# Kernel tuning notes

Hardware: AMD Instinct MI355X
Metric: run time of the kernel (lower is better)

## Reference

```python
import jax, jax.numpy as jnp
import numpy as np

B, S, D, H = 8, 1024, 1024, 16
DH = D // H


def setup_inputs() -> dict:
    key = jax.random.key(0)
    ks = jax.random.split(key, 7)
    scale = 1.0 / np.sqrt(DH)
    return {
        "sequences": jax.random.normal(ks[0], (B, S, D), dtype=jnp.float32),
        "Wq": jax.random.uniform(ks[1], (H, DH, DH), jnp.float32, -scale, scale),
        "bq": jax.random.uniform(ks[2], (H, DH), jnp.float32, -scale, scale),
        "Wk": jax.random.uniform(ks[3], (H, DH, DH), jnp.float32, -scale, scale),
        "bk": jax.random.uniform(ks[4], (H, DH), jnp.float32, -scale, scale),
        "Wv": jax.random.uniform(ks[5], (H, DH, DH), jnp.float32, -scale, scale),
        "bv": jax.random.uniform(ks[6], (H, DH), jnp.float32, -scale, scale),
    }


def reference(sequences, Wq, bq, Wk, bk, Wv, bv):
    # split channels into heads: [B,S,H,DH]
    x = sequences.reshape(B, S, H, DH)
    # per-head linear maps (torch Linear: y = x @ W.T + b)
    q = jnp.einsum("bshd,hed->bshe", x, Wq) + bq  # [B,S,H,DH]
    k = jnp.einsum("bshd,hed->bshe", x, Wk) + bk
    v = jnp.einsum("bshd,hed->bshe", x, Wv) + bv
    scores = jnp.einsum("bshd,bthd->bhst", q, k) / jnp.sqrt(jnp.asarray(DH, x.dtype))
    attn = jax.nn.softmax(scores, axis=-1)  # [B,H,S,S]
    out = jnp.einsum("bhst,bthd->bshd", attn, v)  # [B,S,H,DH]
    return out.reshape(B, S, D)
```

## Files before the change

kernel.cpp:

```cpp
#include <hip/hip_runtime.h>
#include <hip/hip_bf16.h>


constexpr int NB = 8, NS = 1024, ND = 1024, NH = 16, NDH = 64;

typedef __bf16 bf16x8 __attribute__((ext_vector_type(8)));
typedef float f32x4 __attribute__((ext_vector_type(4)));

__device__ __forceinline__ f32x4 mfma16(bf16x8 a, bf16x8 b, f32x4 c) {
  return __builtin_amdgcn_mfma_f32_16x16x32_bf16(a, b, c, 0, 0, 0);
}

__device__ __forceinline__ float fast_exp2(float x) {
#if __has_builtin(__builtin_amdgcn_exp2f)
  return __builtin_amdgcn_exp2f(x);
#else
  return __builtin_exp2f(x);
#endif
}

__device__ __forceinline__ unsigned pack2(float lo, float hi) {
  unsigned uh = __builtin_bit_cast(unsigned, hi) + 0x8000u;
  unsigned ul = __builtin_bit_cast(unsigned, lo) + 0x8000u;
  return __builtin_amdgcn_perm(uh, ul, 0x07060302u);
}

__device__ __forceinline__ unsigned pack2t(float lo, float hi) {
  return __builtin_amdgcn_perm(__builtin_bit_cast(unsigned, hi),
                               __builtin_bit_cast(unsigned, lo), 0x07060302u);
}

__device__ __forceinline__ bf16x8 cvt2bf8(float4 lo, float4 hi) {
  bf16x8 r;
  r[0] = (__bf16)lo.x; r[1] = (__bf16)lo.y; r[2] = (__bf16)lo.z; r[3] = (__bf16)lo.w;
  r[4] = (__bf16)hi.x; r[5] = (__bf16)hi.y; r[6] = (__bf16)hi.z; r[7] = (__bf16)hi.w;
  return r;
}

__device__ __forceinline__ void gload16(const __hip_bfloat16* g, __hip_bfloat16* l) {
  __builtin_amdgcn_global_load_lds(
      (const __attribute__((address_space(1))) void*)g,
      (__attribute__((address_space(3))) void*)l, 16, 0, 0);
}

__global__ __launch_bounds__(256) void qkv_proj_kernel(
    const float* __restrict__ x,
    const float* __restrict__ Wq, const float* __restrict__ bq,
    const float* __restrict__ Wk, const float* __restrict__ bk,
    const float* __restrict__ Wv, const float* __restrict__ bv,
    __hip_bfloat16* __restrict__ Qo, __hip_bfloat16* __restrict__ Ko,
    __hip_bfloat16* __restrict__ Vt) {
  __shared__ __align__(16) __hip_bfloat16 Wlds[3][NDH][72];
  const int tid = threadIdx.x;
  const int wave = tid >> 6, lane = tid & 63;
  const int m = lane & 15, quad = lane >> 4;
  const int h = blockIdx.x & (NH - 1);
  const int sblk = blockIdx.x >> 4;

  const float* Ws[3] = {Wq + h * 4096, Wk + h * 4096, Wv + h * 4096};
#pragma unroll
  for (int mt = 0; mt < 3; mt++) {
#pragma unroll
    for (int p = 0; p < 4; p++) {
      int idx = (p * 256 + tid) * 4;
      float4 v = *(const float4*)(Ws[mt] + idx);
      uint2 w;
      w.x = pack2(v.x, v.y);
      w.y = pack2(v.z, v.w);
      *(uint2*)&Wlds[mt][idx >> 6][idx & 63] = w;
    }
  }
  __syncthreads();

  float bq4[4][4], bk4[4][4], bvv[4];
#pragma unroll
  for (int nt = 0; nt < 4; nt++) {
    float4 a = *(const float4*)(bq + h * 64 + nt * 16 + quad * 4);
    float4 c = *(const float4*)(bk + h * 64 + nt * 16 + quad * 4);
    bq4[nt][0] = a.x; bq4[nt][1] = a.y; bq4[nt][2] = a.z; bq4[nt][3] = a.w;
    bk4[nt][0] = c.x; bk4[nt][1] = c.y; bk4[nt][2] = c.z; bk4[nt][3] = c.w;
    bvv[nt] = bv[h * 64 + nt * 16 + m];
  }

  const int rowbase = sblk * 256 + wave * 64;
  bf16x8 Xf[4][2];
#pragma unroll
  for (int st = 0; st < 4; st++) {
    const float* xp = x + (size_t)(rowbase + st * 16 + m) * ND + h * NDH + quad * 8;
#pragma unroll
    for (int c = 0; c < 2; c++) {
      float4 lo = *(const float4*)(xp + c * 32);
      float4 hi = *(const float4*)(xp + c * 32 + 4);
      Xf[st][c] = cvt2bf8(lo, hi);
    }
  }

  const int b = rowbase >> 10;
  const int s0 = rowbase & 1023;
  const float qscale = 0.18033688011112042f;

#pragma unroll
  for (int mt = 0; mt < 3; mt++) {
#pragma unroll
    for (int nt = 0; nt < 4; nt++) {
      bf16x8 w0 = *(const bf16x8*)&Wlds[mt][nt * 16 + m][quad * 8];
      bf16x8 w1 = *(const bf16x8*)&Wlds[mt][nt * 16 + m][32 + quad * 8];
#pragma unroll
      for (int st = 0; st < 4; st++) {
        f32x4 acc = {0.f, 0.f, 0.f, 0.f};
        if (mt < 2) {
          acc = mfma16(w0, Xf[st][0], acc);
          acc = mfma16(w1, Xf[st][1], acc);
          const int srow = s0 + st * 16 + m;
          uint2 w;
          if (mt == 0) {
            w.x = pack2((acc[0] + bq4[nt][0]) * qscale, (acc[1] + bq4[nt][1]) * qscale);
            w.y = pack2((acc[2] + bq4[nt][2]) * qscale, (acc[3] + bq4[nt][3]) * qscale);
            *(uint2*)(Qo + ((size_t)(b * NH + h) * NS + srow) * NDH +
                      nt * 16 + quad * 4) = w;
          } else {
            w.x = pack2(acc[0] + bk4[nt][0], acc[1] + bk4[nt][1]);
            w.y = pack2(acc[2] + bk4[nt][2], acc[3] + bk4[nt][3]);
            *(uint2*)(Ko + ((size_t)(b * NH + h) * NS + srow) * NDH +
                      nt * 16 + quad * 4) = w;
          }
        } else {
          acc = mfma16(Xf[st][0], w0, acc);
          acc = mfma16(Xf[st][1], w1, acc);
          uint2 w;
          w.x = pack2(acc[0] + bvv[nt], acc[1] + bvv[nt]);
          w.y = pack2(acc[2] + bvv[nt], acc[3] + bvv[nt]);
          *(uint2*)(Vt + ((size_t)(b * NH + h) * NDH + nt * 16 + m) * NS + s0 +
                    st * 16 + quad * 4) = w;
        }
      }
    }
  }
}

__global__ __launch_bounds__(256, 4) void attn_kernel(
    const __hip_bfloat16* __restrict__ Q,
    const __hip_bfloat16* __restrict__ K,
    const __hip_bfloat16* __restrict__ Vt,
    float* __restrict__ out) {
  __shared__ __align__(16) __hip_bfloat16 Kt[2][64][64];
  __shared__ __align__(16) __hip_bfloat16 Vl[2][64][64];

  const int tid = threadIdx.x;
  const int wave = tid >> 6, lane = tid & 63;
  const int m = lane & 15, quad = lane >> 4;

  const int xcd = blockIdx.x & 7;
  const int j = blockIdx.x >> 3;
  const int bh = xcd * 16 + (j & 15);
  const int qblk = j >> 4;
  const int qbase = qblk * 128 + wave * 32;

  const __hip_bfloat16* Qp = Q + (size_t)bh * NS * NDH;
  const __hip_bfloat16* Kp = K + (size_t)bh * NS * NDH;
  const __hip_bfloat16* Vp = Vt + (size_t)bh * NDH * NS;

  bf16x8 Bq[2][2];
#pragma unroll
  for (int g = 0; g < 2; g++)
#pragma unroll
    for (int dh = 0; dh < 2; dh++)
      Bq[g][dh] = *(const bf16x8*)(Qp + (size_t)(qbase + g * 16 + m) * NDH +
                                   dh * 32 + quad * 8);

  f32x4 accO[2][4];
  f32x4 lsum[2];
#pragma unroll
  for (int g = 0; g < 2; g++) {
    lsum[g] = (f32x4){0.f, 0.f, 0.f, 0.f};
#pragma unroll
    for (int nt = 0; nt < 4; nt++) accO[g][nt] = (f32x4){0.f, 0.f, 0.f, 0.f};
  }
  bf16x8 ones8;
#pragma unroll
  for (int i = 0; i < 8; i++) ones8[i] = (__bf16)1.0f;
  const f32x4 fzero = {0.f, 0.f, 0.f, 0.f};

  const int krow = 8 * (m >> 2) + (m & 3);
  const int fK = (m & 3) ^ (((m >> 2) & 1) << 2);
  const int kc0 = (quad ^ fK) * 8;
  const int vbase = quad ^ (m & 7);

#define STAGE(buf, tb)                                                        \
  {                                                                           \
    _Pragma("unroll") for (int l = 0; l < 2; l++) {                           \
      const int krb = wave * 16 + l * 8;                                      \
      const int csK = (lane & 7) ^ ((lane >> 3) & 3) ^ (l << 2);              \
      gload16(Kp + (size_t)((tb) * 64 + krb + (lane >> 3)) * NDH + csK * 8,   \
              &Kt[buf][krb][0]);                                              \
      const int vrb = wave * 16 + l * 8;                                      \
      const int csV = (lane & 7) ^ (lane >> 3);                               \
      gload16(Vp + (size_t)(vrb + (lane >> 3)) * NS + (tb) * 64 + csV * 8,    \
              &Vl[buf][vrb][0]);                                              \
    }                                                                         \
  }

  STAGE(0, 0);

  for (int tb = 0; tb < 16; tb++) {
    const int cur = tb & 1;
    __syncthreads();
    if (tb + 1 < 16) STAGE(cur ^ 1, tb + 1);

    bf16x8 Pa[2][2];
#pragma unroll
    for (int c = 0; c < 2; c++) {
      uint4 u[2];
#pragma unroll
      for (int p = 0; p < 2; p++) {
        const __hip_bfloat16* kr = &Kt[cur][c * 32 + 4 * p + krow][0];
        bf16x8 k0 = *(const bf16x8*)(kr + kc0);
        bf16x8 k1 = *(const bf16x8*)(kr + (kc0 ^ 32));
#pragma unroll
        for (int g = 0; g < 2; g++) {
          f32x4 a = mfma16(k1, Bq[g][1], mfma16(k0, Bq[g][0], fzero));
          unsigned w0 = pack2t(fast_exp2(a[0]), fast_exp2(a[1]));
          unsigned w1 = pack2t(fast_exp2(a[2]), fast_exp2(a[3]));
          if (p == 0) { u[g].x = w0; u[g].y = w1; }
          else        { u[g].z = w0; u[g].w = w1; }
        }
      }
#pragma unroll
      for (int g = 0; g < 2; g++) Pa[g][c] = __builtin_bit_cast(bf16x8, u[g]);
    }
    __builtin_amdgcn_s_setprio(1);
#pragma unroll
    for (int g = 0; g < 2; g++)
#pragma unroll
      for (int c = 0; c < 2; c++) lsum[g] = mfma16(Pa[g][c], ones8, lsum[g]);
#pragma unroll
    for (int nt = 0; nt < 4; nt++) {
#pragma unroll
      for (int c = 0; c < 2; c++) {
        const int off = (vbase ^ (c << 2)) << 3;
        bf16x8 v = *(const bf16x8*)&Vl[cur][nt * 16 + m][off];
#pragma unroll
        for (int g = 0; g < 2; g++)
          accO[g][nt] = mfma16(Pa[g][c], v, accO[g][nt]);
      }
    }
    __builtin_amdgcn_s_setprio(0);
  }
#undef STAGE

  const int b = bh >> 4, h = bh & (NH - 1);
#pragma unroll
  for (int g = 0; g < 2; g++) {
#pragma unroll
    for (int r = 0; r < 4; r++) {
      float inv = 1.0f / lsum[g][r];
      int srow = qbase + g * 16 + quad * 4 + r;
      float* op = out + (size_t)(b * NS + srow) * ND + h * NDH;
#pragma unroll
      for (int nt = 0; nt < 4; nt++) op[nt * 16 + m] = accO[g][nt][r] * inv;
    }
  }
}

extern "C" void kernel_launch(void* const* d_in, const int* in_sizes, int n_in,
                              void* d_out, int out_size, void* d_ws, size_t ws_size,
                              hipStream_t stream) {
  const float* x  = (const float*)d_in[0];
  const float* Wq = (const float*)d_in[1];
  const float* bq = (const float*)d_in[2];
  const float* Wk = (const float*)d_in[3];
  const float* bk = (const float*)d_in[4];
  const float* Wv = (const float*)d_in[5];
  const float* bv = (const float*)d_in[6];
  float* out = (float*)d_out;

  const size_t elems = (size_t)NB * NH * NS * NDH;
  __hip_bfloat16* Qw = (__hip_bfloat16*)d_ws;
  __hip_bfloat16* Kw = Qw + elems;
  __hip_bfloat16* Vw = Kw + elems;

  qkv_proj_kernel<<<512, 256, 0, stream>>>(x, Wq, bq, Wk, bk, Wv, bv, Qw, Kw, Vw);
  attn_kernel<<<1024, 256, 0, stream>>>(Qw, Kw, Vw, out);
}
```

Baseline: 141.4 us.

## Software-pipeline attention loop: overlap QK of next tile with PV of previous

Restructures the attention main loop so each tile's QK^T and exp phase runs while the PV accumulation consumes the previous tile's probabilities. The loop is unrolled by two with ping-pong probability registers, and V is triple-buffered in shared memory so it is not overwritten while still being read. The goal is to interleave exp/VALU work with MFMA work and hide shared-memory load latency. In exchange it holds more live registers, which can hurt occupancy under the 4-block launch bound, uses more LDS, and drops the s_setprio hints.

```diff
diff --git a/kernel.cpp b/kernel.cpp
--- a/kernel.cpp
+++ b/kernel.cpp
@@ -144,7 +144,7 @@
     const __hip_bfloat16* __restrict__ Vt,
     float* __restrict__ out) {
   __shared__ __align__(16) __hip_bfloat16 Kt[2][64][64];
-  __shared__ __align__(16) __hip_bfloat16 Vl[2][64][64];
+  __shared__ __align__(16) __hip_bfloat16 Vl[3][64][64];
 
   const int tid = threadIdx.x;
   const int wave = tid >> 6, lane = tid & 63;
@@ -186,67 +186,74 @@
   const int kc0 = (quad ^ fK) * 8;
   const int vbase = quad ^ (m & 7);
 
-#define STAGE(buf, tb)                                                        \
+#define STAGE(kb, vb, tb)                                                     \
   {                                                                           \
     _Pragma("unroll") for (int l = 0; l < 2; l++) {                           \
       const int krb = wave * 16 + l * 8;                                      \
       const int csK = (lane & 7) ^ ((lane >> 3) & 3) ^ (l << 2);              \
       gload16(Kp + (size_t)((tb) * 64 + krb + (lane >> 3)) * NDH + csK * 8,   \
-              &Kt[buf][krb][0]);                                              \
+              &Kt[kb][krb][0]);                                               \
       const int vrb = wave * 16 + l * 8;                                      \
       const int csV = (lane & 7) ^ (lane >> 3);                               \
       gload16(Vp + (size_t)(vrb + (lane >> 3)) * NS + (tb) * 64 + csV * 8,    \
-              &Vl[buf][vrb][0]);                                              \
+              &Vl[vb][vrb][0]);                                               \
     }                                                                         \
   }
 
-  STAGE(0, 0);
-
-  for (int tb = 0; tb < 16; tb++) {
-    const int cur = tb & 1;
+#define QK_PHASE(cur_, PaNew)                                                 \
+  {                                                                           \
+    _Pragma("unroll") for (int c = 0; c < 2; c++) {                           \
+      uint4 u[2];                                                             \
+      _Pragma("unroll") for (int p = 0; p < 2; p++) {                         \
+        const __hip_bfloat16* kr = &Kt[cur_][c * 32 + 4 * p + krow][0];       \
+        bf16x8 k0 = *(const bf16x8*)(kr + kc0);                               \
+        bf16x8 k1 = *(const bf16x8*)(kr + (kc0 ^ 32));                        \
+        _Pragma("unroll") for (int g = 0; g < 2; g++) {                       \
+          f32x4 a = mfma16(k1, Bq[g][1], mfma16(k0, Bq[g][0], fzero));        \
+          unsigned w0 = pack2t(fast_exp2(a[0]), fast_exp2(a[1]));             \
+          unsigned w1 = pack2t(fast_exp2(a[2]), fast_exp2(a[3]));             \
+          if (p == 0) { u[g].x = w0; u[g].y = w1; }                           \
+          else        { u[g].z = w0; u[g].w = w1; }                           \
+        }                                                                     \
+      }                                                                       \
+      _Pragma("unroll") for (int g = 0; g < 2; g++)                           \
+        PaNew[g][c] = __builtin_bit_cast(bf16x8, u[g]);                       \
+    }                                                                         \
+  }
+
+#define PV_PHASE(vbuf_, PaOld)                                                \
+  {                                                                           \
+    _Pragma("unroll") for (int g = 0; g < 2; g++)                             \
+      _Pragma("unroll") for (int c = 0; c < 2; c++)                           \
+        lsum[g] = mfma16(PaOld[g][c], ones8, lsum[g]);                        \
+    _Pragma("unroll") for (int nt = 0; nt < 4; nt++) {                        \
+      _Pragma("unroll") for (int c = 0; c < 2; c++) {                         \
+        const int off = (vbase ^ (c << 2)) << 3;                              \
+        bf16x8 v = *(const bf16x8*)&Vl[vbuf_][nt * 16 + m][off];              \
+        _Pragma("unroll") for (int g = 0; g < 2; g++)                         \
+          accO[g][nt] = mfma16(PaOld[g][c], v, accO[g][nt]);                  \
+      }                                                                       \
+    }                                                                         \
+  }
+
+  STAGE(0, 0, 0);
+
+  bf16x8 PaA[2][2], PaB[2][2];
+
+  for (int tb2 = 0; tb2 < 16; tb2 += 2) {
     __syncthreads();
-    if (tb + 1 < 16) STAGE(cur ^ 1, tb + 1);
-
-    bf16x8 Pa[2][2];
-#pragma unroll
-    for (int c = 0; c < 2; c++) {
-      uint4 u[2];
-#pragma unroll
-      for (int p = 0; p < 2; p++) {
-        const __hip_bfloat16* kr = &Kt[cur][c * 32 + 4 * p + krow][0];
-        bf16x8 k0 = *(const bf16x8*)(kr + kc0);
-        bf16x8 k1 = *(const bf16x8*)(kr + (kc0 ^ 32));
-#pragma unroll
-        for (int g = 0; g < 2; g++) {
-          f32x4 a = mfma16(k1, Bq[g][1], mfma16(k0, Bq[g][0], fzero));
-          unsigned w0 = pack2t(fast_exp2(a[0]), fast_exp2(a[1]));
-          unsigned w1 = pack2t(fast_exp2(a[2]), fast_exp2(a[3]));
-          if (p == 0) { u[g].x = w0; u[g].y = w1; }
-          else        { u[g].z = w0; u[g].w = w1; }
-        }
-      }
-#pragma unroll
-      for (int g = 0; g < 2; g++) Pa[g][c] = __builtin_bit_cast(bf16x8, u[g]);
-    }
-    __builtin_amdgcn_s_setprio(1);
-#pragma unroll
-    for (int g = 0; g < 2; g++)
-#pragma unroll
-      for (int c = 0; c < 2; c++) lsum[g] = mfma16(Pa[g][c], ones8, lsum[g]);
-#pragma unroll
-    for (int nt = 0; nt < 4; nt++) {
-#pragma unroll
-      for (int c = 0; c < 2; c++) {
-        const int off = (vbase ^ (c << 2)) << 3;
-        bf16x8 v = *(const bf16x8*)&Vl[cur][nt * 16 + m][off];
-#pragma unroll
-        for (int g = 0; g < 2; g++)
-          accO[g][nt] = mfma16(Pa[g][c], v, accO[g][nt]);
-      }
-    }
-    __builtin_amdgcn_s_setprio(0);
-  }
+    STAGE(1, (tb2 + 1) % 3, tb2 + 1);
+    QK_PHASE(0, PaA);
+    if (tb2 > 0) PV_PHASE((tb2 + 2) % 3, PaB);
+    __syncthreads();
+    if (tb2 + 2 < 16) STAGE(0, (tb2 + 2) % 3, tb2 + 2);
+    QK_PHASE(1, PaB);
+    PV_PHASE(tb2 % 3, PaA);
+  }
+  PV_PHASE(0, PaB);
 #undef STAGE
+#undef QK_PHASE
+#undef PV_PHASE
 
   const int b = bh >> 4, h = bh & (NH - 1);
 #pragma unroll
```

Result: slower. 153.4 us (+8.5%).
